# Optimization experiments

Hardware: AMD Instinct MI355X
Metric: run time of the kernel (lower is better)

The kernel has to match this reference:

```python
import jax, jax.numpy as jnp
import numpy as np

DIM = 768
HIDDEN = 4 * DIM          # shared expert hidden
NUM_EXPERTS = 8
TOPK = 2
D_LOW = DIM // 4          # 192


def setup_inputs() -> dict:
    key = jax.random.key(0)
    ks = jax.random.split(key, 8)
    B, C, H, W = 8, DIM, 32, 32
    x = jax.random.normal(ks[0], (B, C, H, W), dtype=jnp.float32)
    # shared expert (1x1 convs == per-pixel linear)
    w1 = jax.random.normal(ks[1], (HIDDEN, DIM), dtype=jnp.float32) * 0.02
    b1 = jnp.zeros((HIDDEN,), dtype=jnp.float32)
    w2 = jax.random.normal(ks[2], (DIM, HIDDEN), dtype=jnp.float32) * 0.02
    b2 = jnp.zeros((DIM,), dtype=jnp.float32)
    # router params (torch Linear weight layout [out, in])
    w_down = jax.random.normal(ks[3], (NUM_EXPERTS * D_LOW, DIM), dtype=jnp.float32) * 0.02
    router_w = jax.random.normal(ks[4], (1, D_LOW), dtype=jnp.float32) * 0.02
    w_up = jax.random.normal(ks[5], (NUM_EXPERTS, D_LOW, DIM), dtype=jnp.float32) * 0.02
    return {"x": x, "w1": w1, "b1": b1, "w2": w2, "b2": b2,
            "w_down": w_down, "router_w": router_w, "w_up": w_up}


def _gelu(v):
    # torch nn.GELU default = exact erf variant
    return jax.nn.gelu(v, approximate=False)


def reference(x, w1, b1, w2, b2, w_down, router_w, w_up):
    B, C, H, W = x.shape
    # ---- shared expert: conv1x1 -> GELU -> conv1x1 ----
    h = jnp.einsum('bchw,oc->bohw', x, w1) + b1[None, :, None, None]
    shared = jnp.einsum('bohw,co->bchw', _gelu(h), w2) + b2[None, :, None, None]
    # ---- AoE router over tokens ----
    N = H * W
    x_flat = x.reshape(B, C, N).transpose(0, 2, 1).reshape(B * N, C)  # [T, C]
    feats = (x_flat @ w_down.T).reshape(-1, NUM_EXPERTS, D_LOW)       # [T, E, d_low]
    logits = jnp.einsum('ted,d->te', feats, router_w[0])              # [T, E]
    probs = jax.nn.softmax(logits, axis=-1)
    topk_w, topk_i = jax.lax.top_k(probs, TOPK)                       # [T, k]
    topk_w = topk_w / jnp.sum(topk_w, axis=-1, keepdims=True)
    sel = jnp.take_along_axis(feats, topk_i[:, :, None], axis=1)      # [T, k, d_low]
    act = _gelu(sel)
    sel_w_up = w_up[topk_i]                                           # [T, k, d_low, C]
    expert_out = jnp.einsum('tkd,tkdm->tkm', act, sel_w_up)           # [T, k, C]
    weighted = jnp.sum(expert_out * topk_w[:, :, None], axis=1)       # [T, C]
    # aux load-balance loss
    mean_prob = jnp.mean(probs, axis=0)
    one_hot = jnp.sum(jax.nn.one_hot(topk_i, NUM_EXPERTS, dtype=probs.dtype), axis=1)
    mean_load = jnp.mean(one_hot, axis=0)
    aux_loss = NUM_EXPERTS * jnp.sum(mean_prob * mean_load)
    aoe = weighted.reshape(B, N, C).transpose(0, 2, 1).reshape(B, C, H, W)
    return x + shared + aoe, aux_loss
```

## Files before the change

### kernel.cpp

```cpp
#include <hip/hip_runtime.h>
#include <cstdint>
#include <cmath>

#define DIM   768
#define HID   3072
#define NEXP  8
#define DLOW  192
#define NPB   1024
#define NTOK  8192
#define KD    1536
#define KCAT  4608

typedef unsigned short ushort_t;
typedef short   short8  __attribute__((ext_vector_type(8)));
typedef float   float4v __attribute__((ext_vector_type(4)));

__device__ inline ushort_t f2b(float f) {
    union { float f; unsigned int i; } v; v.f = f;
    unsigned int x = v.i;
    return (ushort_t)((x + 0x7fffu + ((x >> 16) & 1u)) >> 16);
}
__device__ inline float gelu_fast(float x) {
    const float z = 1.5957691216057308f * x * __builtin_fmaf(0.044715f * x, x, 1.0f);
    return x * __builtin_amdgcn_rcpf(1.0f + __expf(-z));
}

__device__ __forceinline__ void async_ld16(const ushort_t* g, ushort_t* l) {
    __builtin_amdgcn_global_load_lds(
        (const __attribute__((address_space(1))) void*)g,
        (__attribute__((address_space(3))) void*)l,
        16, 0, 0);
}


__global__ __launch_bounds__(256, 2)
void gemm_in(const ushort_t* __restrict__ A, const ushort_t* __restrict__ B,
             ushort_t* __restrict__ Cb, const float* __restrict__ bias,
             const int* __restrict__ tokE, const float* __restrict__ tokW,
             const float* __restrict__ accbuf, float* __restrict__ outAux,
             int m_base)
{
    __shared__ __align__(16) ushort_t As[2 * 128 * 64];
    __shared__ __align__(16) ushort_t Bs[2 * 128 * 64];

    const int tid  = threadIdx.x;
    const int lane = tid & 63;
    const int wave = tid >> 6;
    const int quad = lane >> 4;
    const int l16  = lane & 15;
    const int wm   = (wave >> 1) * 64;
    const int wn   = (wave & 1) * 64;

    const int bid = blockIdx.y * gridDim.x + blockIdx.x;
    const int mpx = gridDim.y >> 3;
    const int xcd = bid & 7;
    const int loc = bid >> 3;
    const int m0  = (xcd * mpx + loc % mpx) * 128;
    const int n0  = (loc / mpx) * 128;

    float4v acc[4][4];
#pragma unroll
    for (int i = 0; i < 4; i++)
#pragma unroll
        for (int j = 0; j < 4; j++) acc[i][j] = (float4v)0.0f;

    const ushort_t* ga[4]; ushort_t* la[4];
#pragma unroll
    for (int j = 0; j < 4; j++) {
        const int f = j * 256 + tid;
        const int mm = f >> 3;
        const int gs = ((f & 7) ^ (mm & 7)) * 8;
        ga[j] = A + (size_t)(m0 + mm) * DIM + gs;
        la[j] = &As[f * 8];
    }
    const ushort_t* gb[4]; ushort_t* lb[4];
#pragma unroll
    for (int j = 0; j < 4; j++) {
        const int f = j * 256 + tid;
        const int mm = f >> 3;
        const int gs = ((f & 7) ^ (mm & 7)) * 8;
        gb[j] = B + (size_t)(n0 + mm) * DIM + gs;
        lb[j] = &Bs[f * 8];
    }

    const ushort_t* pa[2][4]; const ushort_t* pb[2][4];
#pragma unroll
    for (int kh = 0; kh < 2; kh++)
#pragma unroll
        for (int i = 0; i < 4; i++) {
            const int ra = wm + i * 16 + l16;
            pa[kh][i] = &As[ra * 64 + (((quad + 4 * kh) ^ (ra & 7)) * 8)];
            const int rb = wn + i * 16 + l16;
            pb[kh][i] = &Bs[rb * 64 + (((quad + 4 * kh) ^ (rb & 7)) * 8)];
        }

#define STG_I(k0, ao, bo) do {                                              \
    _Pragma("unroll")                                                       \
    for (int j = 0; j < 4; j++) async_ld16(ga[j] + (k0), la[j] + (ao));     \
    _Pragma("unroll")                                                       \
    for (int j = 0; j < 4; j++) async_ld16(gb[j] + (k0), lb[j] + (bo)); } while (0)

#define BODY_I(t, ao, bo) do {                                              \
    short8 af0[4], bv0[4], af1[4], bv1[4];                                  \
    _Pragma("unroll")                                                       \
    for (int i = 0; i < 4; i++) {                                           \
        af0[i] = *(const short8*)(pa[0][i] + (ao));                         \
        af1[i] = *(const short8*)(pa[1][i] + (ao));                         \
        bv0[i] = *(const short8*)(pb[0][i] + (bo));                         \
        bv1[i] = *(const short8*)(pb[1][i] + (bo));                         \
    }                                                                       \
    asm volatile("s_waitcnt lgkmcnt(0)" ::: "memory");                      \
    __builtin_amdgcn_sched_barrier(0);                                      \
    __builtin_amdgcn_s_barrier();           \
    __builtin_amdgcn_sched_barrier(0);          \
    const bool st_ = (t) + 2 < 12;                                          \
    if (st_) STG_I(((t) + 2) * 64, ao, bo);                                 \
    __builtin_amdgcn_s_setprio(1);                                          \
    _Pragma("unroll")                                                       \
    for (int im = 0; im < 4; im++)                                          \
        _Pragma("unroll")                                                   \
        for (int in = 0; in < 4; in++)                                      \
            acc[im][in] = __builtin_amdgcn_mfma_f32_16x16x32_bf16(          \
                af0[im], bv0[in], acc[im][in], 0, 0, 0);                    \
    _Pragma("unroll")                                                       \
    for (int im = 0; im < 4; im++)                                          \
        _Pragma("unroll")                                                   \
        for (int in = 0; in < 4; in++)                                      \
            acc[im][in] = __builtin_amdgcn_mfma_f32_16x16x32_bf16(          \
                af1[im], bv1[in], acc[im][in], 0, 0, 0);                    \
    __builtin_amdgcn_s_setprio(0);                                          \
    if (st_) asm volatile("s_waitcnt vmcnt(8)" ::: "memory");               \
    else     asm volatile("s_waitcnt vmcnt(0)" ::: "memory");               \
    __builtin_amdgcn_sched_barrier(0);                                      \
    __builtin_amdgcn_s_barrier();             \
    __builtin_amdgcn_sched_barrier(0);                                      \
} while (0)

    STG_I(0, 0, 0);
    STG_I(64, 128 * 64, 128 * 64);
    asm volatile("s_waitcnt vmcnt(8)" ::: "memory");
    __builtin_amdgcn_s_barrier();
    __builtin_amdgcn_sched_barrier(0);

    for (int tt = 0; tt < 12; tt += 2) {
        BODY_I(tt, 0, 0);
        BODY_I(tt + 1, 128 * 64, 128 * 64);
    }
#undef STG_I
#undef BODY_I

    if (n0 < HID) {
#pragma unroll
        for (int in = 0; in < 4; in++) {
            const int col = n0 + wn + in * 16 + l16;
            const float bvv = bias[col];
#pragma unroll
            for (int im = 0; im < 4; im++) {
                const int rowl = m0 + wm + im * 16 + quad * 4;
#pragma unroll
                for (int r = 0; r < 4; r++)
                    Cb[(size_t)(rowl + r) * KCAT + col] =
                        f2b(gelu_fast(acc[im][in][r] + bvv));
            }
        }
        if (m_base == 0 && blockIdx.x == 0 && blockIdx.y == 0 && tid == 0) {
            float aux = 0.0f;
            for (int e = 0; e < 8; e++) aux += accbuf[e] * accbuf[8 + e];
            outAux[0] = aux * 8.0f / ((float)NTOK * (float)NTOK);
        }
    } else {
        int eidx[4];
#pragma unroll
        for (int in = 0; in < 4; in++)
            eidx[in] = (n0 + wn + in * 16 - HID) / DLOW;
#pragma unroll
        for (int im = 0; im < 4; im++) {
            const int rowl = m0 + wm + im * 16 + quad * 4;
#pragma unroll
            for (int r = 0; r < 4; r++) {
                const int g = m_base + rowl + r;
                const int e0 = tokE[2 * g], e1 = tokE[2 * g + 1];
                const float w0 = tokW[2 * g], w1 = tokW[2 * g + 1];
#pragma unroll
                for (int in = 0; in < 4; in++) {
                    const int col = n0 + wn + in * 16 + l16;
                    const float m = (eidx[in] == e0) ? w0
                                  : ((eidx[in] == e1) ? w1 : 0.0f);
                    Cb[(size_t)(rowl + r) * KCAT + col] =
                        f2b(gelu_fast(acc[im][in][r]) * m);
                }
            }
        }
    }
}

__global__ __launch_bounds__(256, 2)
void gemm_out(const ushort_t* __restrict__ A, const ushort_t* __restrict__ B,
              float* __restrict__ out, const float* __restrict__ bias,
              const float* __restrict__ X, int m_base)
{
    __shared__ __align__(16) ushort_t As[2 * 128 * 64];
    __shared__ __align__(16) ushort_t Bs[2 * 96 * 64];

    const int tid  = threadIdx.x;
    const int lane = tid & 63;
    const int wave = tid >> 6;
    const int quad = lane >> 4;
    const int l16  = lane & 15;
    const int wm   = (wave >> 1) * 64;
    const int wn   = (wave & 1) * 48;

    const int nwg = gridDim.x * gridDim.y;
    const int bid = blockIdx.y * gridDim.x + blockIdx.x;
    const int swz = (bid & 7) * (nwg >> 3) + (bid >> 3);
    const int m0  = (swz / gridDim.x) * 128;
    const int n0  = (swz % gridDim.x) * 96;

    float4v acc[4][3];
#pragma unroll
    for (int i = 0; i < 4; i++)
#pragma unroll
        for (int j = 0; j < 3; j++) acc[i][j] = (float4v)0.0f;

    const ushort_t* ga[4]; ushort_t* la[4];
#pragma unroll
    for (int j = 0; j < 4; j++) {
        const int f = j * 256 + tid;
        const int mm = f >> 3;
        const int gs = ((f & 7) ^ (mm & 7)) * 8;
        ga[j] = A + (size_t)(m0 + mm) * KCAT + gs;
        la[j] = &As[f * 8];
    }
    const ushort_t* gb[3]; ushort_t* lb[3];
#pragma unroll
    for (int j = 0; j < 3; j++) {
        const int f = j * 256 + tid;
        const int mm = f >> 3;
        const int gs = ((f & 7) ^ (mm & 7)) * 8;
        gb[j] = B + (size_t)(n0 + mm) * KCAT + gs;
        lb[j] = &Bs[f * 8];
    }

    const ushort_t* pa[2][4]; const ushort_t* pb[2][3];
#pragma unroll
    for (int kh = 0; kh < 2; kh++) {
#pragma unroll
        for (int i = 0; i < 4; i++) {
            const int ra = wm + i * 16 + l16;
            pa[kh][i] = &As[ra * 64 + (((quad + 4 * kh) ^ (ra & 7)) * 8)];
        }
#pragma unroll
        for (int i = 0; i < 3; i++) {
            const int rb = wn + i * 16 + l16;
            pb[kh][i] = &Bs[rb * 64 + (((quad + 4 * kh) ^ (rb & 7)) * 8)];
        }
    }

#define STG_O(k0, ao, bo) do {                                              \
    _Pragma("unroll")                                                       \
    for (int j = 0; j < 4; j++) async_ld16(ga[j] + (k0), la[j] + (ao));     \
    _Pragma("unroll")                                                       \
    for (int j = 0; j < 3; j++) async_ld16(gb[j] + (k0), lb[j] + (bo)); } while (0)

#define BODY_O(t, ao, bo) do {                                              \
    short8 af0[4], bv0[3], af1[4], bv1[3];                                  \
    _Pragma("unroll")                                                       \
    for (int i = 0; i < 4; i++) {                                           \
        af0[i] = *(const short8*)(pa[0][i] + (ao));                         \
        af1[i] = *(const short8*)(pa[1][i] + (ao));                         \
    }                                                                       \
    _Pragma("unroll")                                                       \
    for (int i = 0; i < 3; i++) {                                           \
        bv0[i] = *(const short8*)(pb[0][i] + (bo));                         \
        bv1[i] = *(const short8*)(pb[1][i] + (bo));                         \
    }                                                                       \
    asm volatile("s_waitcnt lgkmcnt(0)" ::: "memory");                      \
    __builtin_amdgcn_sched_barrier(0);                                      \
    __builtin_amdgcn_s_barrier();           \
    __builtin_amdgcn_sched_barrier(0);          \
    const bool st_ = (t) + 2 < 72;                                          \
    if (st_) STG_O(((t) + 2) * 64, ao, bo);                                 \
    __builtin_amdgcn_s_setprio(1);                                          \
    _Pragma("unroll")                                                       \
    for (int im = 0; im < 4; im++)                                          \
        _Pragma("unroll")                                                   \
        for (int in = 0; in < 3; in++)                                      \
            acc[im][in] = __builtin_amdgcn_mfma_f32_16x16x32_bf16(          \
                af0[im], bv0[in], acc[im][in], 0, 0, 0);                    \
    _Pragma("unroll")                                                       \
    for (int im = 0; im < 4; im++)                                          \
        _Pragma("unroll")                                                   \
        for (int in = 0; in < 3; in++)                                      \
            acc[im][in] = __builtin_amdgcn_mfma_f32_16x16x32_bf16(          \
                af1[im], bv1[in], acc[im][in], 0, 0, 0);                    \
    __builtin_amdgcn_s_setprio(0);                                          \
    if (st_) asm volatile("s_waitcnt vmcnt(7)" ::: "memory");               \
    else     asm volatile("s_waitcnt vmcnt(0)" ::: "memory");               \
    __builtin_amdgcn_sched_barrier(0);                                      \
    __builtin_amdgcn_s_barrier();             \
    __builtin_amdgcn_sched_barrier(0);                                      \
} while (0)

    STG_O(0, 0, 0);
    STG_O(64, 128 * 64, 96 * 64);
    asm volatile("s_waitcnt vmcnt(7)" ::: "memory");
    __builtin_amdgcn_s_barrier();
    __builtin_amdgcn_sched_barrier(0);

    for (int tt = 0; tt < 72; tt += 2) {
        BODY_O(tt, 0, 0);
        BODY_O(tt + 1, 128 * 64, 96 * 64);
    }
#undef STG_O
#undef BODY_O

#pragma unroll
    for (int in = 0; in < 3; in++) {
        const int col = n0 + wn + in * 16 + l16;
        const float bvv = bias[col];
#pragma unroll
        for (int im = 0; im < 4; im++) {
            const int grow = m_base + m0 + wm + im * 16 + quad * 4;
            const int bb = grow >> 10, nn = grow & 1023;
            const size_t base = ((size_t)bb * DIM + col) * NPB + nn;
            const float4 xv = *(const float4*)(X + base);
            float4 v;
            v.x = acc[im][in][0] + bvv + xv.x;
            v.y = acc[im][in][1] + bvv + xv.y;
            v.z = acc[im][in][2] + bvv + xv.z;
            v.w = acc[im][in][3] + bvv + xv.w;
            *(float4*)(out + base) = v;
        }
    }
}

#define NB_TX   1536
#define NB_WUP  1152
#define NB_W2   (DIM * HID / 4 / 256)
#define NB_WIN  (KCAT * DIM / 4 / 256)
#define NB_WEFF (NEXP * DIM / 256)
#define NB_PREP (NB_TX + NB_WUP + NB_W2 + NB_WIN + NB_WEFF)

__global__ __launch_bounds__(256)
void prep_all(const float* __restrict__ x,  ushort_t* __restrict__ XT,
              const float* __restrict__ wup, ushort_t* __restrict__ Wcat,
              const float* __restrict__ w2,  const float* __restrict__ w1,
              const float* __restrict__ wdn, ushort_t* __restrict__ Win,
              const float* __restrict__ rw,  float* __restrict__ Weff,
              float* __restrict__ accb)
{
    __shared__ ushort_t tile[32][33];
    __shared__ __align__(16) ushort_t t2[64 * 68];
    const int tid = threadIdx.x;
    const int tx = tid & 31, ty = tid >> 5;
    int blk = blockIdx.x;

    if (blk < NB_TX) {
        const int bx = blk & 15;
        const int rest = blk >> 4;
        const int by = rest % 12, b = rest / 12;
        const int n0 = bx * 64, c0 = by * 64;
#pragma unroll
        for (int j = 0; j < 4; j++) {
            const int idx = j * 256 + tid;
            const int c = idx >> 4, q = idx & 15;
            const float4 v = *(const float4*)(
                x + ((size_t)b * DIM + c0 + c) * NPB + n0 + 4 * q);
            uint2 p;
            p.x = (unsigned)f2b(v.x) | ((unsigned)f2b(v.y) << 16);
            p.y = (unsigned)f2b(v.z) | ((unsigned)f2b(v.w) << 16);
            *(uint2*)&t2[c * 68 + 4 * q] = p;
        }
        __syncthreads();
#pragma unroll
        for (int j = 0; j < 2; j++) {
            const int w = (tid >> 3) + 32 * j;
            const int p = tid & 7;
            ushort_t u[8];
#pragma unroll
            for (int cc = 0; cc < 8; cc++) u[cc] = t2[(8 * p + cc) * 68 + w];
            uint4 o;
            o.x = (unsigned)u[0] | ((unsigned)u[1] << 16);
            o.y = (unsigned)u[2] | ((unsigned)u[3] << 16);
            o.z = (unsigned)u[4] | ((unsigned)u[5] << 16);
            o.w = (unsigned)u[6] | ((unsigned)u[7] << 16);
            *(uint4*)&XT[((size_t)b * NPB + n0 + w) * DIM + c0 + 8 * p] = o;
        }
        return;
    }
    blk -= NB_TX;
    if (blk < NB_WUP) {
        const int bx = blk % 24, by = blk / 24;
        const int c0 = bx * 32, k0 = by * 32;
#pragma unroll
        for (int j = 0; j < 4; j++)
            tile[ty + 8 * j][tx] =
                f2b(wup[(size_t)(k0 + ty + 8 * j) * DIM + c0 + tx]);
        __syncthreads();
#pragma unroll
        for (int j = 0; j < 4; j++)
            Wcat[(size_t)(c0 + ty + 8 * j) * KCAT + HID + k0 + tx] =
                tile[tx][ty + 8 * j];
        return;
    }
    blk -= NB_WUP;
    if (blk < NB_W2) {
        const int i = blk * 256 + tid;
        const int c = i / (HID / 4), h = (i % (HID / 4)) * 4;
        const float4 v = *(const float4*)(w2 + (size_t)c * HID + h);
        uint2 p;
        p.x = (unsigned)f2b(v.x) | ((unsigned)f2b(v.y) << 16);
        p.y = (unsigned)f2b(v.z) | ((unsigned)f2b(v.w) << 16);
        *(uint2*)(Wcat + (size_t)c * KCAT + h) = p;
        return;
    }
    blk -= NB_W2;
    if (blk < NB_WIN) {
        const int i = blk * 256 + tid;
        const int n1 = HID * DIM / 4;
        const float4 v = (i < n1) ? ((const float4*)w1)[i]
                                  : ((const float4*)wdn)[i - n1];
        uint2 p;
        p.x = (unsigned)f2b(v.x) | ((unsigned)f2b(v.y) << 16);
        p.y = (unsigned)f2b(v.z) | ((unsigned)f2b(v.w) << 16);
        ((uint2*)Win)[i] = p;
        return;
    }
    blk -= NB_WIN;
    {
        const int idx = blk * 256 + tid;
        const int e = idx / DIM, c = idx % DIM;
        float s = 0.0f;
        for (int d = 0; d < DLOW; d++)
            s += wdn[(size_t)(e * DLOW + d) * DIM + c] * rw[d];
        Weff[idx] = s;
        if (blk == 0 && tid < 16) accb[tid] = 0.0f;
    }
}

__global__ __launch_bounds__(256)
void router_kernel(const float* __restrict__ x, const float* __restrict__ Weff,
                   int* __restrict__ tokE, float* __restrict__ tokW,
                   float* __restrict__ accbuf)
{
    __shared__ float sW[NEXP * DIM];
    __shared__ float sAcc[16];
    const int tid = threadIdx.x;
    for (int i = tid; i < NEXP * DIM; i += 256) sW[i] = Weff[i];
    if (tid < 16) sAcc[tid] = 0.0f;
    __syncthreads();

    const int t = blockIdx.x * 256 + tid;
    const int b = t >> 10, n = t & 1023;
    const float* xb = x + (size_t)b * DIM * NPB + n;

    float lg[8];
#pragma unroll
    for (int e = 0; e < 8; e++) lg[e] = 0.0f;
#pragma unroll 8
    for (int c = 0; c < DIM; c++) {
        const float xv = xb[(size_t)c * NPB];
#pragma unroll
        for (int e = 0; e < 8; e++) lg[e] += xv * sW[e * DIM + c];
    }

    float mx = lg[0];
#pragma unroll
    for (int e = 1; e < 8; e++) mx = fmaxf(mx, lg[e]);
    float pr[8], s = 0.0f;
#pragma unroll
    for (int e = 0; e < 8; e++) { pr[e] = expf(lg[e] - mx); s += pr[e]; }
    const float inv = 1.0f / s;
#pragma unroll
    for (int e = 0; e < 8; e++) pr[e] *= inv;
    int e0 = 0;
#pragma unroll
    for (int e = 1; e < 8; e++) if (pr[e] > pr[e0]) e0 = e;
    int e1 = (e0 == 0) ? 1 : 0;
#pragma unroll
    for (int e = 0; e < 8; e++) if (e != e0 && pr[e] > pr[e1]) e1 = e;
    const float wsum = pr[e0] + pr[e1];
    tokE[2 * t + 0] = e0;  tokE[2 * t + 1] = e1;
    tokW[2 * t + 0] = pr[e0] / wsum;  tokW[2 * t + 1] = pr[e1] / wsum;

#pragma unroll
    for (int e = 0; e < 8; e++) atomicAdd(&sAcc[e], pr[e]);
    atomicAdd(&sAcc[8 + e0], 1.0f);
    atomicAdd(&sAcc[8 + e1], 1.0f);
    __syncthreads();
    if (tid < 16) atomicAdd(&accbuf[tid], sAcc[tid]);
}

extern "C" void kernel_launch(void* const* d_in, const int* in_sizes, int n_in,
                              void* d_out, int out_size, void* d_ws, size_t ws_size,
                              hipStream_t stream)
{
    (void)in_sizes; (void)n_in; (void)out_size;

    const float* x   = (const float*)d_in[0];
    const float* w1  = (const float*)d_in[1];
    const float* b1  = (const float*)d_in[2];
    const float* w2  = (const float*)d_in[3];
    const float* b2  = (const float*)d_in[4];
    const float* wdn = (const float*)d_in[5];
    const float* rw  = (const float*)d_in[6];
    const float* wup = (const float*)d_in[7];
    float* out = (float*)d_out;

    char* ws = (char*)d_ws;
    size_t off = 0;
    ushort_t* XTbf = (ushort_t*)(ws + off); off += (size_t)NTOK * DIM * 2;
    ushort_t* Win  = (ushort_t*)(ws + off); off += (size_t)KCAT * DIM * 2;
    ushort_t* Wcat = (ushort_t*)(ws + off); off += (size_t)DIM * KCAT * 2;
    float*    Weff = (float*)  (ws + off);  off += (size_t)NEXP * DIM * 4;
    int*      tokE = (int*)    (ws + off);  off += (size_t)NTOK * 2 * 4;
    float*    tokW = (float*)  (ws + off);  off += (size_t)NTOK * 2 * 4;
    float*    accb = (float*)  (ws + off);  off += 256;

    int chunk = NTOK / 4;
    if      (ws_size >= off + (size_t)NTOK * KCAT * 2)       chunk = NTOK;
    else if (ws_size >= off + (size_t)(NTOK / 2) * KCAT * 2) chunk = NTOK / 2;
    ushort_t* HU = (ushort_t*)(ws + off);

    prep_all<<<NB_PREP, 256, 0, stream>>>(x, XTbf, wup, Wcat, w2, w1, wdn,
                                          Win, rw, Weff, accb);
    router_kernel<<<NTOK / 256, 256, 0, stream>>>(x, Weff, tokE, tokW, accb);

    for (int c = 0; c < NTOK / chunk; c++) {
        const ushort_t* Ax = XTbf + (size_t)c * chunk * DIM;
        const int m_base = c * chunk;
        gemm_in<<<dim3(KCAT / 128, chunk / 128), 256, 0, stream>>>(
            Ax, Win, HU, b1, tokE, tokW, accb, out + (size_t)NTOK * DIM, m_base);
        gemm_out<<<dim3(DIM / 96, chunk / 128), 256, 0, stream>>>(
            HU, Wcat, out, b2, x, m_base);
    }
}
```

Baseline: 306.5 us.

## Software-pipeline LDS fragment loads with MFMA halves in first GEMM

Restructures the first GEMM main loop so the second K-half fragments load from LDS while the first-half MFMAs run, and the next tile's first-half fragments are prefetched after the barrier, overlapping them with the second-half MFMAs. It removes the exposed LDS-read latency before each MFMA block. The loop is now fully unrolled over 12 steps, which increases code size. The prefetched fragments are held across the barrier, which adds register pressure.

```diff
diff --git a/kernel.cpp b/kernel.cpp
--- a/kernel.cpp
+++ b/kernel.cpp
@@ -100,54 +100,63 @@
     _Pragma("unroll")                                                       \
     for (int j = 0; j < 4; j++) async_ld16(gb[j] + (k0), lb[j] + (bo)); } while (0)
 
-#define BODY_I(t, ao, bo) do {                                              \
-    short8 af0[4], bv0[4], af1[4], bv1[4];                                  \
-    _Pragma("unroll")                                                       \
-    for (int i = 0; i < 4; i++) {                                           \
-        af0[i] = *(const short8*)(pa[0][i] + (ao));                         \
-        af1[i] = *(const short8*)(pa[1][i] + (ao));                         \
-        bv0[i] = *(const short8*)(pb[0][i] + (bo));                         \
-        bv1[i] = *(const short8*)(pb[1][i] + (bo));                         \
-    }                                                                       \
-    asm volatile("s_waitcnt lgkmcnt(0)" ::: "memory");                      \
-    __builtin_amdgcn_sched_barrier(0);                                      \
-    __builtin_amdgcn_s_barrier();           \
-    __builtin_amdgcn_sched_barrier(0);          \
-    const bool st_ = (t) + 2 < 12;                                          \
-    if (st_) STG_I(((t) + 2) * 64, ao, bo);                                 \
-    __builtin_amdgcn_s_setprio(1);                                          \
-    _Pragma("unroll")                                                       \
-    for (int im = 0; im < 4; im++)                                          \
-        _Pragma("unroll")                                                   \
-        for (int in = 0; in < 4; in++)                                      \
-            acc[im][in] = __builtin_amdgcn_mfma_f32_16x16x32_bf16(          \
-                af0[im], bv0[in], acc[im][in], 0, 0, 0);                    \
-    _Pragma("unroll")                                                       \
-    for (int im = 0; im < 4; im++)                                          \
-        _Pragma("unroll")                                                   \
-        for (int in = 0; in < 4; in++)                                      \
-            acc[im][in] = __builtin_amdgcn_mfma_f32_16x16x32_bf16(          \
-                af1[im], bv1[in], acc[im][in], 0, 0, 0);                    \
-    __builtin_amdgcn_s_setprio(0);                                          \
-    if (st_) asm volatile("s_waitcnt vmcnt(8)" ::: "memory");               \
-    else     asm volatile("s_waitcnt vmcnt(0)" ::: "memory");               \
-    __builtin_amdgcn_sched_barrier(0);                                      \
-    __builtin_amdgcn_s_barrier();             \
-    __builtin_amdgcn_sched_barrier(0);                                      \
-} while (0)
+    short8 afH[2][4], bvH[2][4];
 
     STG_I(0, 0, 0);
     STG_I(64, 128 * 64, 128 * 64);
     asm volatile("s_waitcnt vmcnt(8)" ::: "memory");
     __builtin_amdgcn_s_barrier();
     __builtin_amdgcn_sched_barrier(0);
-
-    for (int tt = 0; tt < 12; tt += 2) {
-        BODY_I(tt, 0, 0);
-        BODY_I(tt + 1, 128 * 64, 128 * 64);
+#pragma unroll
+    for (int i = 0; i < 4; i++) {
+        afH[0][i] = *(const short8*)(pa[0][i]);
+        bvH[0][i] = *(const short8*)(pb[0][i]);
+    }
+
+#pragma unroll
+    for (int t = 0; t < 12; ++t) {
+        const int co = (t & 1) * (128 * 64);
+        const int no = ((t + 1) & 1) * (128 * 64);
+
+#pragma unroll
+        for (int i = 0; i < 4; i++) {
+            afH[1][i] = *(const short8*)(pa[1][i] + co);
+            bvH[1][i] = *(const short8*)(pb[1][i] + co);
+        }
+#pragma unroll
+        for (int im = 0; im < 4; im++)
+#pragma unroll
+            for (int in = 0; in < 4; in++)
+                acc[im][in] = __builtin_amdgcn_mfma_f32_16x16x32_bf16(
+                    afH[0][im], bvH[0][in], acc[im][in], 0, 0, 0);
+        asm volatile("s_waitcnt lgkmcnt(0)" ::: "memory");
+        __builtin_amdgcn_sched_barrier(0);
+        __builtin_amdgcn_s_barrier();
+        __builtin_amdgcn_sched_barrier(0);
+        if (t + 2 < 12) {
+            STG_I((t + 2) * 64, co, co);
+            asm volatile("s_waitcnt vmcnt(8)" ::: "memory");
+        } else {
+            asm volatile("s_waitcnt vmcnt(0)" ::: "memory");
+        }
+        __builtin_amdgcn_sched_barrier(0);
+        __builtin_amdgcn_s_barrier();
+        __builtin_amdgcn_sched_barrier(0);
+        if (t + 1 < 12) {
+#pragma unroll
+            for (int i = 0; i < 4; i++) {
+                afH[0][i] = *(const short8*)(pa[0][i] + no);
+                bvH[0][i] = *(const short8*)(pb[0][i] + no);
+            }
+        }
+#pragma unroll
+        for (int im = 0; im < 4; im++)
+#pragma unroll
+            for (int in = 0; in < 4; in++)
+                acc[im][in] = __builtin_amdgcn_mfma_f32_16x16x32_bf16(
+                    afH[1][im], bvH[1][in], acc[im][in], 0, 0, 0);
     }
 #undef STG_I
-#undef BODY_I
 
     if (n0 < HID) {
 #pragma unroll
```

Result: no change. 306.5 us (+0.0%).
